# Kernel tuning notes

Hardware: AMD Instinct MI355X
Metric: run time of the kernel (lower is better)

The kernel has to match this reference:

```python
import jax, jax.numpy as jnp
import numpy as np

EPS = 1e-5
GRID = 128          # coarse grid extent -> fine grid is 256^3
N1 = 15000          # coarse voxels
CHILD = 4           # children kept per coarse voxel
N2 = N1 * CHILD     # fine voxels
CIN = 128
COUT = 64


def _build_geometry():
    rng = np.random.RandomState(0)
    flat = rng.choice(GRID ** 3, N1, replace=False)
    cc = np.stack(np.unravel_index(flat, (GRID, GRID, GRID)), axis=1)  # [N1,3]
    offs8 = np.array([[i, j, k] for i in (0, 1) for j in (0, 1) for k in (0, 1)], dtype=np.int64)
    kidx = np.argsort(rng.rand(N1, 8), axis=1)[:, :CHILD]              # [N1,4] distinct child taps
    fine = (cc[:, None, :] * 2 + offs8[kidx]).reshape(-1, 3)           # [N2,3] unique fine coords
    up_src = np.repeat(np.arange(N1), CHILD).astype(np.int32)
    up_kidx = kidx.reshape(-1).astype(np.int32)
    # 27-offset neighbor maps via hashed coordinate lookup
    key = (fine[:, 0] * 256 + fine[:, 1]) * 256 + fine[:, 2]
    order = np.argsort(key)
    skey = key[order]
    offs27 = np.array([[i, j, k] for i in (-1, 0, 1) for j in (-1, 0, 1) for k in (-1, 0, 1)], dtype=np.int64)
    nbr_src = np.full((27, N2), N2, dtype=np.int32)
    nbr_dst = np.full((27, N2), N2, dtype=np.int32)
    for t in range(27):
        q = fine + offs27[t]
        inb = np.all((q >= 0) & (q < 256), axis=1)
        qk = (q[:, 0] * 256 + q[:, 1]) * 256 + q[:, 2]
        pos = np.searchsorted(skey, qk)
        pos = np.clip(pos, 0, N2 - 1)
        hit = inb & (skey[pos] == qk)
        nbr_src[t, hit] = order[pos[hit]]
        nbr_dst[t, hit] = np.arange(N2, dtype=np.int32)[hit]
    return up_src, up_kidx, nbr_src, nbr_dst


def setup_inputs() -> dict:
    key = jax.random.key(0)
    ks = jax.random.split(key, 8)
    up_src, up_kidx, nbr_src, nbr_dst = _build_geometry()
    s_up = 1.0 / np.sqrt(CIN * 8)
    s1 = 1.0 / np.sqrt(CIN * 27)
    s2 = 1.0 / np.sqrt(COUT * 27)
    return {
        "feats1": jax.random.normal(ks[0], (N1, CIN), jnp.float32),
        "feats2": jax.random.normal(ks[1], (N2, CIN // 2), jnp.float32),
        "w_up": jax.random.normal(ks[2], (8, CIN, CIN // 2), jnp.float32) * s_up,
        "gamma_up": jnp.ones((CIN // 2,), jnp.float32),
        "beta_up": jnp.zeros((CIN // 2,), jnp.float32),
        "w1": jax.random.normal(ks[3], (27, CIN, COUT), jnp.float32) * s1,
        "gamma1": jnp.ones((COUT,), jnp.float32),
        "beta1": jnp.zeros((COUT,), jnp.float32),
        "w2": jax.random.normal(ks[4], (27, COUT, COUT), jnp.float32) * s2,
        "gamma2": jnp.ones((COUT,), jnp.float32),
        "beta2": jnp.zeros((COUT,), jnp.float32),
        "up_src": jnp.asarray(up_src),
        "up_kidx": jnp.asarray(up_kidx),
        "nbr_src": jnp.asarray(nbr_src),
        "nbr_dst": jnp.asarray(nbr_dst),
    }


def _bn_relu(x, gamma, beta):
    # training-mode BatchNorm over the point dimension (biased variance), then ReLU
    m = jnp.mean(x, axis=0)
    v = jnp.var(x, axis=0)
    return jax.nn.relu((x - m) * jax.lax.rsqrt(v + EPS) * gamma + beta)


def _sparse_conv(x, w, nbr_src, nbr_dst):
    # x: [N,Ci]; w: [27,Ci,Co]; transform-then-gather-scatter (hash-map sparse conv)
    n = x.shape[0]
    co = w.shape[-1]
    y = jnp.einsum("nc,kco->kno", x, w)                       # [27,N,Co]
    y = jnp.concatenate([y, jnp.zeros((27, 1, co), y.dtype)], axis=1)  # sentinel row
    msg = jnp.take_along_axis(y, nbr_src[:, :, None], axis=1)  # [27,N,Co]
    out = jnp.zeros((n + 1, co), y.dtype).at[nbr_dst.reshape(-1)].add(msg.reshape(-1, co))
    return out[:-1]


def reference(feats1, feats2, w_up, gamma_up, beta_up, w1, gamma1, beta1, w2,
              gamma2, beta2, up_src, up_kidx, nbr_src, nbr_dst):
    # transposed conv k=2 s=2, generative=False: each fine voxel pulls from its unique coarse parent
    y = jnp.einsum("mc,kco->kmo", feats1, w_up)               # [8,N1,Cin/2]
    x1 = y[up_kidx, up_src]                                   # [N2,Cin/2]
    x1 = _bn_relu(x1, gamma_up, beta_up)
    x = jnp.concatenate([x1, feats2], axis=-1)                # [N2,Cin]
    h = _bn_relu(_sparse_conv(x, w1, nbr_src, nbr_dst), gamma1, beta1)
    return _bn_relu(_sparse_conv(h, w2, nbr_src, nbr_dst), gamma2, beta2)
```

## Files before the change

kernel.cpp:

```cpp
#include <hip/hip_runtime.h>


typedef short bf16x4 __attribute__((ext_vector_type(4)));
typedef short bf16x8 __attribute__((ext_vector_type(8)));
typedef float f32x16 __attribute__((ext_vector_type(16)));

#define ROWM 0xFFFFF
#define RFLAG (1 << 30)

__device__ __forceinline__ short f2bf(float f) {
    unsigned u = __float_as_uint(f);
    u += 0x7fffu + ((u >> 16) & 1u);
    return (short)(u >> 16);
}
__device__ __forceinline__ float bf2f(short s) {
    return __uint_as_float(((unsigned)(unsigned short)s) << 16);
}

__global__ __launch_bounds__(256) void k_setup(
    const float* __restrict__ w_up, const float* __restrict__ f1,
    const int* __restrict__ up_kidx,
    short* __restrict__ wupp, short* __restrict__ f1bf,
    int* __restrict__ pmask, int* __restrict__ perm_rows,
    int* __restrict__ rank, int* __restrict__ cnt,
    int n1, int nbGeom)
{
    int tid = threadIdx.x;
    int bid = blockIdx.x;
    if (bid < nbGeom) {
        int p = bid * 256 + tid;
        if (p >= n1) return;
        int4 kd = *(const int4*)(up_kidx + 4 * p);
        int a = kd.x * 4 + 0, b = kd.y * 4 + 1, c = kd.z * 4 + 2, d = kd.w * 4 + 3;
        int t;
        if (a > b) { t = a; a = b; b = t; }
        if (c > d) { t = c; c = d; d = t; }
        if (a > c) { t = a; a = c; c = t; }
        if (b > d) { t = b; b = d; d = t; }
        if (b > c) { t = b; b = c; c = t; }
        perm_rows[4 * p + 0] = 4 * p + (a & 3);
        perm_rows[4 * p + 1] = 4 * p + (b & 3);
        perm_rows[4 * p + 2] = 4 * p + (c & 3);
        perm_rows[4 * p + 3] = 4 * p + (d & 3);
        int mask = (1 << (a >> 2)) | (1 << (b >> 2)) | (1 << (c >> 2)) | (1 << (d >> 2));
        pmask[p] = mask;
        rank[p] = atomicAdd(&cnt[mask], 1);
    } else {
        const int nup8 = 8192;
        int tot = nup8 + n1 * 16;
        int gs = (gridDim.x - nbGeom) * 256;
        for (int e8 = (bid - nbGeom) * 256 + tid; e8 < tot; e8 += gs) {
            if (e8 < nup8) {
                int l = e8 & 63, nt = (e8 >> 6) & 15, ks = e8 >> 10;
                int kb = ks * 16 + (l >> 5) * 8;
                int col = nt * 32 + (l & 31);
                const float* src = w_up + (size_t)(col >> 6) * 8192 + (size_t)kb * 64 + (col & 63);
                bf16x8 o;
                #pragma unroll
                for (int j = 0; j < 8; ++j) o[j] = f2bf(src[(size_t)j * 64]);
                *(bf16x8*)(wupp + (size_t)e8 * 8) = o;
            } else {
                int g = e8 - nup8;
                const float* src = f1 + (size_t)g * 8;
                float4 a = *(const float4*)src;
                float4 b = *(const float4*)(src + 4);
                bf16x8 o;
                o[0] = f2bf(a.x); o[1] = f2bf(a.y); o[2] = f2bf(a.z); o[3] = f2bf(a.w);
                o[4] = f2bf(b.x); o[5] = f2bf(b.y); o[6] = f2bf(b.z); o[7] = f2bf(b.w);
                *(bf16x8*)(f1bf + (size_t)g * 8) = o;
            }
        }
    }
}

__global__ __launch_bounds__(256) void k_up(
    const short* __restrict__ f1bf, const short* __restrict__ wupp,
    const int* __restrict__ pmask, const int* __restrict__ cnt,
    const int* __restrict__ rank, int* __restrict__ perm_par,
    int4* __restrict__ tiles, int* __restrict__ ntl,
    short* __restrict__ yup8, float* __restrict__ stats,
    const float* __restrict__ w1, const float* __restrict__ w2,
    short* __restrict__ w1p, short* __restrict__ w2p,
    const int* __restrict__ nbr, int2* __restrict__ ext,
    int* __restrict__ extc, unsigned* __restrict__ flagbits,
    float* __restrict__ y1, float* __restrict__ y2,
    int n1, int n2, int nt, int nbExt)
{
    int gemmEnd = 1 + 2 * nt;
    if (blockIdx.x == 0) {
        __shared__ int sA[256], sB[256], bb[256];
        int t = threadIdx.x;
        int c = cnt[t], tc = (c + 31) >> 5;
        sA[t] = c; sB[t] = tc;
        __syncthreads();
        for (int off = 1; off < 256; off <<= 1) {
            int a = (t >= off) ? sA[t - off] : 0;
            int b = (t >= off) ? sB[t - off] : 0;
            __syncthreads();
            sA[t] += a; sB[t] += b;
            __syncthreads();
        }
        int base = sA[t] - c, toff = sB[t] - tc;
        bb[t] = base;
        for (int j = 0; j < tc; ++j) tiles[toff + j] = make_int4(t, base, j * 32, c);
        if (t == 255) ntl[0] = sB[255];
        __syncthreads();
        for (int p = t; p < n1; p += 256)
            perm_par[bb[pmask[p]] + rank[p]] = p;
        return;
    }
    if (blockIdx.x >= gemmEnd) {
        int ab = blockIdx.x - gemmEnd;
        int tid = threadIdx.x;
        if (ab < 256) {
            long long tot = (long long)n2 * 16;
            float4 z = make_float4(0.f, 0.f, 0.f, 0.f);
            for (long long e = (long long)ab * 256 + tid; e < tot; e += 256LL * 256) {
                ((float4*)y1)[e] = z;
                ((float4*)y2)[e] = z;
            }
        } else if (ab < 320) {
            const int nw18 = 27648, tot = 27648 + 13824;
            for (int e8 = (ab - 256) * 256 + tid; e8 < tot; e8 += 64 * 256) {
                if (e8 < nw18) {
                    int l = e8 & 63, ch = (e8 >> 6) & 1, ks = (e8 >> 7) & 7, t = e8 >> 10;
                    int kb = ks * 16 + (l >> 5) * 8;
                    int col = ch * 32 + (l & 31);
                    const float* src = w1 + (size_t)t * 8192 + (size_t)kb * 64 + col;
                    bf16x8 o;
                    #pragma unroll
                    for (int j = 0; j < 8; ++j) o[j] = f2bf(src[(size_t)j * 64]);
                    *(bf16x8*)(w1p + (size_t)e8 * 8) = o;
                } else {
                    int g = e8 - nw18;
                    int l = g & 63, ch = (g >> 6) & 1, ks = (g >> 7) & 3, t = g >> 9;
                    int kb = ks * 16 + (l >> 5) * 8;
                    int col = ch * 32 + (l & 31);
                    const float* src = w2 + (size_t)t * 4096 + (size_t)kb * 64 + col;
                    bf16x8 o;
                    #pragma unroll
                    for (int j = 0; j < 8; ++j) o[j] = f2bf(src[(size_t)j * 64]);
                    *(bf16x8*)(w2p + (size_t)g * 8) = o;
                }
            }
        } else {
            int i = (ab - 320) * 256 + tid;
            unsigned hm = 0;
            if (i < n2) {
                #pragma unroll
                for (int t = 0; t < 27; ++t) {
                    int s = nbr[(size_t)t * n2 + i];
                    if (s < n2 && (s >> 2) != (i >> 2)) hm |= 1u << t;
                }
            }
            if (hm) atomicOr(&flagbits[i >> 5], 1u << (i & 31));
            __shared__ int lcnt, lbase;
            if (tid == 0) lcnt = 0;
            __syncthreads();
            int nh = __popc(hm);
            int myofs = 0;
            if (nh) myofs = atomicAdd(&lcnt, nh);
            __syncthreads();
            if (tid == 0 && lcnt) lbase = atomicAdd(extc, lcnt);
            __syncthreads();
            if (nh) {
                int pos = lbase + myofs;
                unsigned m = hm;
                while (m) {
                    int t = __ffs(m) - 1;
                    m &= m - 1;
                    int s = nbr[(size_t)t * n2 + i];
                    ext[pos++] = make_int2(i, s | (t << 16));
                }
            }
        }
        return;
    }
    __shared__ short lds[32 * 136];
    __shared__ float bs[64], bq[64];
    int bid = blockIdx.x - 1;
    int tile = bid >> 1;
    int w = threadIdx.x >> 6, lane = threadIdx.x & 63;
    int na = (bid & 1) * 8 + w, nb = na + 4;
    if (threadIdx.x < 64) { bs[threadIdx.x] = 0.f; bq[threadIdx.x] = 0.f; }
    #pragma unroll
    for (int it = 0; it < 2; ++it) {
        int c = it * 256 + threadIdx.x;
        int row = c >> 4, col8 = c & 15;
        int gr = tile * 32 + row; if (gr >= n1) gr = n1 - 1;
        int4 g = *(const int4*)(f1bf + (size_t)gr * 128 + col8 * 8);
        short* d = &lds[row * 136 + col8 * 8];
        *(int2*)d = make_int2(g.x, g.y);
        *(int2*)(d + 4) = make_int2(g.z, g.w);
    }
    int m = lane & 31, half = lane >> 5;
    int pm_l = (tile * 32 + m < n1) ? pmask[tile * 32 + m] : 0;
    __syncthreads();
    f32x16 a0, a1;
    #pragma unroll
    for (int i = 0; i < 16; ++i) { a0[i] = 0.f; a1[i] = 0.f; }
    const bf16x8* bp = (const bf16x8*)wupp;
    #pragma unroll
    for (int ks = 0; ks < 8; ++ks) {
        const short* ap = &lds[m * 136 + ks * 16 + half * 8];
        bf16x4 lo = *(const bf16x4*)ap, hi = *(const bf16x4*)(ap + 4);
        bf16x8 a = __builtin_shufflevector(lo, hi, 0, 1, 2, 3, 4, 5, 6, 7);
        bf16x8 b0 = bp[(size_t)(ks * 16 + na) * 64 + lane];
        bf16x8 b1 = bp[(size_t)(ks * 16 + nb) * 64 + lane];
        a0 = __builtin_amdgcn_mfma_f32_32x32x16_bf16(a, b0, a0, 0, 0, 0);
        a1 = __builtin_amdgcn_mfma_f32_32x32x16_bf16(a, b1, a1, 0, 0, 0);
    }
    int col = lane & 31;
    #pragma unroll
    for (int pass = 0; pass < 2; ++pass) {
        const f32x16& acc = pass ? a1 : a0;
        int n = pass ? nb : na;
        int slot = n >> 1, c = (n & 1) * 32 + col;
        float s0 = 0.f, q0 = 0.f;
        #pragma unroll
        for (int reg = 0; reg < 16; ++reg) {
            int r = (reg & 3) + 8 * (reg >> 2) + 4 * half;
            int p = tile * 32 + r;
            float v = acc[reg];
            int mk = __shfl(pm_l, r);
            if (p < n1) {
                yup8[(size_t)p * 512 + n * 32 + col] = f2bf(v);
                if ((mk >> slot) & 1) { s0 += v; q0 += v * v; }
            }
        }
        s0 += __shfl_xor(s0, 32);
        q0 += __shfl_xor(q0, 32);
        if (lane < 32) { atomicAdd(&bs[c], s0); atomicAdd(&bq[c], q0); }
    }
    __syncthreads();
    if (threadIdx.x < 64) {
        atomicAdd(&stats[threadIdx.x], bs[threadIdx.x]);
        atomicAdd(&stats[64 + threadIdx.x], bq[threadIdx.x]);
    }
}

__device__ __forceinline__ void pair_epi2(const f32x16& a0v, const f32x16& a1v,
                                          int outrow0, int outrow1, int lane,
                                          int ch, float* __restrict__ y,
                                          float* __restrict__ bs,
                                          float* __restrict__ bq)
{
    int col = lane & 31;
    int c = ch * 32 + col;
    float s0 = 0.f, q0 = 0.f;
    #pragma unroll
    for (int reg = 0; reg < 16; ++reg) {
        int r = (reg & 3) + 8 * (reg >> 2) + 4 * (lane >> 5);
        int r0 = __shfl(outrow0, r);
        int r1 = __shfl(outrow1, r);
        if (r0 >= 0) {
            float v = a0v[reg];
            size_t ad = (size_t)(r0 & ROWM) * 64 + c;
            if (r0 & RFLAG) {
                float old = atomicAdd(&y[ad], v);
                s0 += v; q0 += v * (v + 2.f * old);
            } else {
                y[ad] = v; s0 += v; q0 += v * v;
            }
        }
        if (r1 >= 0) {
            float v = a1v[reg];
            size_t ad = (size_t)(r1 & ROWM) * 64 + c;
            if (r1 & RFLAG) {
                float old = atomicAdd(&y[ad], v);
                s0 += v; q0 += v * (v + 2.f * old);
            } else {
                y[ad] = v; s0 += v; q0 += v * v;
            }
        }
    }
    s0 += __shfl_xor(s0, 32);
    q0 += __shfl_xor(q0, 32);
    if (lane < 32) { atomicAdd(&bs[c], s0); atomicAdd(&bq[c], q0); }
}

__device__ __forceinline__ int tap27(int pa, int pb) {
    int di = ((pb >> 2) & 1) - ((pa >> 2) & 1);
    int dj = ((pb >> 1) & 1) - ((pa >> 1) & 1);
    int dk = (pb & 1) - (pa & 1);
    return (di + 1) * 9 + (dj + 1) * 3 + (dk + 1);
}

__global__ __launch_bounds__(256) void k_pairA(
    const short* __restrict__ yup8, const float* __restrict__ f2,
    const int* __restrict__ up_kidx, const short* __restrict__ wp,
    const float* __restrict__ gamma, const float* __restrict__ beta,
    const float* __restrict__ stats, const int* __restrict__ perm_par,
    const int* __restrict__ perm_rows, const int4* __restrict__ tiles,
    const int* __restrict__ n_tiles, const int2* __restrict__ ext,
    const int* __restrict__ extc, const unsigned* __restrict__ flagbits,
    float* __restrict__ y, float* __restrict__ ostats, int n2, int nExtB)
{
    constexpr int LP = 520;
    __shared__ short lds[32 * LP];
    __shared__ int srows[128], soff[128];
    __shared__ float scs[64], shs[64], bs[64], bq[64];
    int tid = threadIdx.x;
    if (blockIdx.x < nExtB) {
        if (tid < 64) {
            float inv = 1.0f / (float)n2;
            float mean = stats[tid] * inv;
            float var = stats[64 + tid] * inv - mean * mean;
            float s = gamma[tid] * rsqrtf(var + 1e-5f);
            scs[tid] = s; shs[tid] = beta[tid] - mean * s;
            bs[tid] = 0.f; bq[tid] = 0.f;
        }
        __syncthreads();
        int gw = (blockIdx.x * 256 + tid) >> 6;
        int nw = nExtB * 4;
        int c = tid & 63;
        int ch = c >> 5, lcol = c & 31;
        int ec = extc[0];
        const bf16x8* wb = (const bf16x8*)wp;
        for (int e = gw; e < ec; e += nw) {
            int2 en = ext[e];
            int i = en.x, s = en.y & 0xFFFF, t = en.y >> 16;
            const short* xr = yup8 + (size_t)(s >> 2) * 512 + up_kidx[s] * 64;
            const float* fr = f2 + (size_t)s * 64;
            float acc = 0.f;
            #pragma unroll
            for (int ks = 0; ks < 8; ++ks) {
                #pragma unroll
                for (int hf = 0; hf < 2; ++hf) {
                    int kb = ks * 16 + hf * 8;
                    float xv[8];
                    if (kb < 64) {
                        bf16x8 g = *(const bf16x8*)(xr + kb);
                        #pragma unroll
                        for (int j = 0; j < 8; ++j)
                            xv[j] = fmaxf(bf2f(g[j]) * scs[kb + j] + shs[kb + j], 0.f);
                    } else {
                        float4 g0 = *(const float4*)(fr + kb - 64);
                        float4 g1 = *(const float4*)(fr + kb - 60);
                        xv[0] = g0.x; xv[1] = g0.y; xv[2] = g0.z; xv[3] = g0.w;
                        xv[4] = g1.x; xv[5] = g1.y; xv[6] = g1.z; xv[7] = g1.w;
                    }
                    bf16x8 wv = wb[((size_t)(t * 8 + ks) * 2 + ch) * 64 + hf * 32 + lcol];
                    #pragma unroll
                    for (int j = 0; j < 8; ++j)
                        acc += xv[j] * bf2f(wv[j]);
                }
            }
            float old = atomicAdd(&y[(size_t)i * 64 + c], acc);
            atomicAdd(&bs[c], acc);
            atomicAdd(&bq[c], acc * (acc + 2.f * old));
        }
        __syncthreads();
        if (tid < 64) {
            atomicAdd(&ostats[tid], bs[tid]);
            atomicAdd(&ostats[64 + tid], bq[tid]);
        }
        return;
    }
    int bt = blockIdx.x - nExtB;
    if (bt >= n_tiles[0]) return;
    int4 td = tiles[bt];
    int mask = td.x, p_start = td.y, lt = td.z, cntb = td.w;
    if (tid < 128) {
        int li = lt + (tid >> 2);
        int pid = perm_par[p_start + ((li < cntb) ? li : 0)];
        int i = perm_rows[pid * 4 + (tid & 3)];
        unsigned fb = (flagbits[i >> 5] >> (i & 31)) & 1u;
        srows[tid] = i | (int)(fb << 30);
        soff[tid] = (i >> 2) * 512 + up_kidx[i] * 64;
    } else if (tid < 192) {
        int cc = tid - 128;
        float inv = 1.0f / (float)n2;
        float mean = stats[cc] * inv;
        float var = stats[64 + cc] * inv - mean * mean;
        float s = gamma[cc] * rsqrtf(var + 1e-5f);
        scs[cc] = s; shs[cc] = beta[cc] - mean * s;
    } else {
        int cc = tid - 192;
        bs[cc] = 0.f; bq[cc] = 0.f;
    }
    __syncthreads();
    #pragma unroll
    for (int it = 0; it < 8; ++it) {
        int c0 = it * 256 + tid;
        int pl = c0 >> 6, w8 = c0 & 63;
        int j = w8 >> 4, col8 = w8 & 15;
        short* d = &lds[pl * LP + j * 128 + col8 * 8];
        if (col8 < 8) {
            bf16x8 g = *(const bf16x8*)(yup8 + (size_t)soff[pl * 4 + j] + col8 * 8);
            short o[8];
            #pragma unroll
            for (int u = 0; u < 8; ++u) {
                int cc = col8 * 8 + u;
                o[u] = f2bf(fmaxf(bf2f(g[u]) * scs[cc] + shs[cc], 0.f));
            }
            *(int2*)d = make_int2(((int)(unsigned short)o[0]) | ((int)o[1] << 16),
                                  ((int)(unsigned short)o[2]) | ((int)o[3] << 16));
            *(int2*)(d + 4) = make_int2(((int)(unsigned short)o[4]) | ((int)o[5] << 16),
                                        ((int)(unsigned short)o[6]) | ((int)o[7] << 16));
        } else {
            const float* fr = f2 + (size_t)(srows[pl * 4 + j] & ROWM) * 64 + (col8 - 8) * 8;
            float4 f0 = *(const float4*)fr;
            float4 f1v = *(const float4*)(fr + 4);
            short o[8] = {f2bf(f0.x), f2bf(f0.y), f2bf(f0.z), f2bf(f0.w),
                          f2bf(f1v.x), f2bf(f1v.y), f2bf(f1v.z), f2bf(f1v.w)};
            *(int2*)d = make_int2(((int)(unsigned short)o[0]) | ((int)o[1] << 16),
                                  ((int)(unsigned short)o[2]) | ((int)o[3] << 16));
            *(int2*)(d + 4) = make_int2(((int)(unsigned short)o[4]) | ((int)o[5] << 16),
                                        ((int)(unsigned short)o[6]) | ((int)o[7] << 16));
        }
    }
    int p0 = -1, p1 = -1, p2 = -1, p3 = -1;
    #pragma unroll
    for (int b = 7; b >= 0; --b)
        if ((mask >> b) & 1) { p3 = p2; p2 = p1; p1 = p0; p0 = b; }
    int w = tid >> 6, lane = tid & 63;
    int a0 = w >> 1, a1 = a0 + 2, ch = w & 1;
    int pa0 = (a0 == 0) ? p0 : p1;
    int pa1 = (a1 == 2) ? p2 : p3;
    int t00 = tap27(pa0, p0), t01 = tap27(pa0, p1), t02 = tap27(pa0, p2), t03 = tap27(pa0, p3);
    int t10 = tap27(pa1, p0), t11 = tap27(pa1, p1), t12 = tap27(pa1, p2), t13 = tap27(pa1, p3);
    int m = lane & 31, half = lane >> 5;
    int li = lt + m;
    bool vp = li < cntb;
    int outrow0 = vp ? srows[m * 4 + a0] : -1;
    int outrow1 = vp ? srows[m * 4 + a1] : -1;
    __syncthreads();
    f32x16 acc0, acc1;
    #pragma unroll
    for (int i = 0; i < 16; ++i) { acc0[i] = 0.f; acc1[i] = 0.f; }
    const bf16x8* bp = (const bf16x8*)wp;
    #pragma unroll
    for (int b = 0; b < 4; ++b) {
        int tb0 = (b == 0) ? t00 : (b == 1) ? t01 : (b == 2) ? t02 : t03;
        int tb1 = (b == 0) ? t10 : (b == 1) ? t11 : (b == 2) ? t12 : t13;
        #pragma unroll
        for (int kk = 0; kk < 8; ++kk) {
            int ks = b * 8 + kk;
            const short* ap = &lds[m * LP + ks * 16 + half * 8];
            bf16x4 lo = *(const bf16x4*)ap, hi = *(const bf16x4*)(ap + 4);
            bf16x8 a = __builtin_shufflevector(lo, hi, 0, 1, 2, 3, 4, 5, 6, 7);
            bf16x8 b0 = bp[((size_t)(tb0 * 8 + kk) * 2 + ch) * 64 + lane];
            bf16x8 b1 = bp[((size_t)(tb1 * 8 + kk) * 2 + ch) * 64 + lane];
            acc0 = __builtin_amdgcn_mfma_f32_32x32x16_bf16(a, b0, acc0, 0, 0, 0);
            acc1 = __builtin_amdgcn_mfma_f32_32x32x16_bf16(a, b1, acc1, 0, 0, 0);
        }
    }
    pair_epi2(acc0, acc1, outrow0, outrow1, lane, ch, y, bs, bq);
    __syncthreads();
    if (tid < 64) {
        atomicAdd(&ostats[tid], bs[tid]);
        atomicAdd(&ostats[64 + tid], bq[tid]);
    }
}

__global__ __launch_bounds__(256) void k_pairB(
    const float* __restrict__ y1, const short* __restrict__ wp,
    const float* __restrict__ gamma, const float* __restrict__ beta,
    const float* __restrict__ stats, const int* __restrict__ perm_par,
    const int* __restrict__ perm_rows, const int4* __restrict__ tiles,
    const int* __restrict__ n_tiles, const int2* __restrict__ ext,
    const int* __restrict__ extc, const unsigned* __restrict__ flagbits,
    float* __restrict__ y, float* __restrict__ ostats, int n2, int nExtB)
{
    constexpr int LP = 264;
    __shared__ short lds[32 * LP];
    __shared__ int srows[128];
    __shared__ float scs[64], shs[64], bs[64], bq[64];
    int tid = threadIdx.x;
    if (blockIdx.x < nExtB) {
        if (tid < 64) {
            float inv = 1.0f / (float)n2;
            float mean = stats[tid] * inv;
            float var = stats[64 + tid] * inv - mean * mean;
            float s = gamma[tid] * rsqrtf(var + 1e-5f);
            scs[tid] = s; shs[tid] = beta[tid] - mean * s;
            bs[tid] = 0.f; bq[tid] = 0.f;
        }
        __syncthreads();
        int gw = (blockIdx.x * 256 + tid) >> 6;
        int nw = nExtB * 4;
        int c = tid & 63;
        int ch = c >> 5, lcol = c & 31;
        int ec = extc[0];
        const bf16x8* wb = (const bf16x8*)wp;
        for (int e = gw; e < ec; e += nw) {
            int2 en = ext[e];
            int i = en.x, s = en.y & 0xFFFF, t = en.y >> 16;
            const float* hr = y1 + (size_t)s * 64;
            float acc = 0.f;
            #pragma unroll
            for (int ks = 0; ks < 4; ++ks) {
                #pragma unroll
                for (int hf = 0; hf < 2; ++hf) {
                    int kb = ks * 16 + hf * 8;
                    float4 g0 = *(const float4*)(hr + kb);
                    float4 g1 = *(const float4*)(hr + kb + 4);
                    float xv[8];
                    xv[0] = g0.x; xv[1] = g0.y; xv[2] = g0.z; xv[3] = g0.w;
                    xv[4] = g1.x; xv[5] = g1.y; xv[6] = g1.z; xv[7] = g1.w;
                    #pragma unroll
                    for (int j = 0; j < 8; ++j)
                        xv[j] = fmaxf(xv[j] * scs[kb + j] + shs[kb + j], 0.f);
                    bf16x8 wv = wb[((size_t)(t * 4 + ks) * 2 + ch) * 64 + hf * 32 + lcol];
                    #pragma unroll
                    for (int j = 0; j < 8; ++j)
                        acc += xv[j] * bf2f(wv[j]);
                }
            }
            float old = atomicAdd(&y[(size_t)i * 64 + c], acc);
            atomicAdd(&bs[c], acc);
            atomicAdd(&bq[c], acc * (acc + 2.f * old));
        }
        __syncthreads();
        if (tid < 64) {
            atomicAdd(&ostats[tid], bs[tid]);
            atomicAdd(&ostats[64 + tid], bq[tid]);
        }
        return;
    }
    int bt = blockIdx.x - nExtB;
    if (bt >= n_tiles[0]) return;
    int4 td = tiles[bt];
    int mask = td.x, p_start = td.y, lt = td.z, cntb = td.w;
    if (tid < 128) {
        int li = lt + (tid >> 2);
        int pid = perm_par[p_start + ((li < cntb) ? li : 0)];
        int i = perm_rows[pid * 4 + (tid & 3)];
        unsigned fb = (flagbits[i >> 5] >> (i & 31)) & 1u;
        srows[tid] = i | (int)(fb << 30);
    } else if (tid < 192) {
        int cc = tid - 128;
        float inv = 1.0f / (float)n2;
        float mean = stats[cc] * inv;
        float var = stats[64 + cc] * inv - mean * mean;
        float s = gamma[cc] * rsqrtf(var + 1e-5f);
        scs[cc] = s; shs[cc] = beta[cc] - mean * s;
    } else {
        int cc = tid - 192;
        bs[cc] = 0.f; bq[cc] = 0.f;
    }
    __syncthreads();
    #pragma unroll
    for (int it = 0; it < 4; ++it) {
        int c0 = it * 256 + tid;
        int pl = c0 >> 5, w8 = c0 & 31;
        int j = w8 >> 3, col8 = w8 & 7;
        const float* fr = y1 + (size_t)(srows[pl * 4 + j] & ROWM) * 64 + col8 * 8;
        float4 f0 = *(const float4*)fr;
        float4 f1v = *(const float4*)(fr + 4);
        short o[8];
        #pragma unroll
        for (int u = 0; u < 4; ++u) {
            int cc = col8 * 8 + u;
            float v = (u == 0) ? f0.x : (u == 1) ? f0.y : (u == 2) ? f0.z : f0.w;
            o[u] = f2bf(fmaxf(v * scs[cc] + shs[cc], 0.f));
        }
        #pragma unroll
        for (int u = 0; u < 4; ++u) {
            int cc = col8 * 8 + 4 + u;
            float v = (u == 0) ? f1v.x : (u == 1) ? f1v.y : (u == 2) ? f1v.z : f1v.w;
            o[4 + u] = f2bf(fmaxf(v * scs[cc] + shs[cc], 0.f));
        }
        short* d = &lds[pl * LP + j * 64 + col8 * 8];
        *(int2*)d = make_int2(((int)(unsigned short)o[0]) | ((int)o[1] << 16),
                              ((int)(unsigned short)o[2]) | ((int)o[3] << 16));
        *(int2*)(d + 4) = make_int2(((int)(unsigned short)o[4]) | ((int)o[5] << 16),
                                    ((int)(unsigned short)o[6]) | ((int)o[7] << 16));
    }
    int p0 = -1, p1 = -1, p2 = -1, p3 = -1;
    #pragma unroll
    for (int b = 7; b >= 0; --b)
        if ((mask >> b) & 1) { p3 = p2; p2 = p1; p1 = p0; p0 = b; }
    int w = tid >> 6, lane = tid & 63;
    int a0 = w >> 1, a1 = a0 + 2, ch = w & 1;
    int pa0 = (a0 == 0) ? p0 : p1;
    int pa1 = (a1 == 2) ? p2 : p3;
    int t00 = tap27(pa0, p0), t01 = tap27(pa0, p1), t02 = tap27(pa0, p2), t03 = tap27(pa0, p3);
    int t10 = tap27(pa1, p0), t11 = tap27(pa1, p1), t12 = tap27(pa1, p2), t13 = tap27(pa1, p3);
    int m = lane & 31, half = lane >> 5;
    int li = lt + m;
    bool vp = li < cntb;
    int outrow0 = vp ? srows[m * 4 + a0] : -1;
    int outrow1 = vp ? srows[m * 4 + a1] : -1;
    __syncthreads();
    f32x16 acc0, acc1;
    #pragma unroll
    for (int i = 0; i < 16; ++i) { acc0[i] = 0.f; acc1[i] = 0.f; }
    const bf16x8* bp = (const bf16x8*)wp;
    #pragma unroll
    for (int b = 0; b < 4; ++b) {
        int tb0 = (b == 0) ? t00 : (b == 1) ? t01 : (b == 2) ? t02 : t03;
        int tb1 = (b == 0) ? t10 : (b == 1) ? t11 : (b == 2) ? t12 : t13;
        #pragma unroll
        for (int kk = 0; kk < 4; ++kk) {
            int ks = b * 4 + kk;
            const short* ap = &lds[m * LP + ks * 16 + half * 8];
            bf16x4 lo = *(const bf16x4*)ap, hi = *(const bf16x4*)(ap + 4);
            bf16x8 a = __builtin_shufflevector(lo, hi, 0, 1, 2, 3, 4, 5, 6, 7);
            bf16x8 b0 = bp[((size_t)(tb0 * 4 + kk) * 2 + ch) * 64 + lane];
            bf16x8 b1 = bp[((size_t)(tb1 * 4 + kk) * 2 + ch) * 64 + lane];
            acc0 = __builtin_amdgcn_mfma_f32_32x32x16_bf16(a, b0, acc0, 0, 0, 0);
            acc1 = __builtin_amdgcn_mfma_f32_32x32x16_bf16(a, b1, acc1, 0, 0, 0);
        }
    }
    pair_epi2(acc0, acc1, outrow0, outrow1, lane, ch, y, bs, bq);
    __syncthreads();
    if (tid < 64) {
        atomicAdd(&ostats[tid], bs[tid]);
        atomicAdd(&ostats[64 + tid], bq[tid]);
    }
}

__global__ __launch_bounds__(256) void k_final(
    const float* __restrict__ y, const float* __restrict__ gamma,
    const float* __restrict__ beta, const float* __restrict__ stats,
    float* __restrict__ out, int n2)
{
    __shared__ float sc[64], sh[64];
    int tid = threadIdx.x;
    if (tid < 64) {
        float inv = 1.0f / (float)n2;
        float mean = stats[tid] * inv;
        float var = stats[64 + tid] * inv - mean * mean;
        float s = gamma[tid] * rsqrtf(var + 1e-5f);
        sc[tid] = s;
        sh[tid] = beta[tid] - mean * s;
    }
    __syncthreads();
    long long total = (long long)n2 * 16;
    long long stride = (long long)gridDim.x * blockDim.x;
    for (long long idx = (long long)blockIdx.x * blockDim.x + tid; idx < total; idx += stride) {
        int i = (int)(idx >> 4);
        int c4 = ((int)idx & 15) * 4;
        const float* src = y + (size_t)i * 64 + c4;
        float4 o;
        o.x = fmaxf(src[0] * sc[c4 + 0] + sh[c4 + 0], 0.f);
        o.y = fmaxf(src[1] * sc[c4 + 1] + sh[c4 + 1], 0.f);
        o.z = fmaxf(src[2] * sc[c4 + 2] + sh[c4 + 2], 0.f);
        o.w = fmaxf(src[3] * sc[c4 + 3] + sh[c4 + 3], 0.f);
        *(float4*)(out + (size_t)i * 64 + c4) = o;
    }
}

extern "C" void kernel_launch(void* const* d_in, const int* in_sizes, int n_in,
                              void* d_out, int out_size, void* d_ws, size_t ws_size,
                              hipStream_t stream)
{
    const float* feats1   = (const float*)d_in[0];
    const float* feats2   = (const float*)d_in[1];
    const float* w_up     = (const float*)d_in[2];
    const float* gamma_up = (const float*)d_in[3];
    const float* beta_up  = (const float*)d_in[4];
    const float* w1       = (const float*)d_in[5];
    const float* gamma1   = (const float*)d_in[6];
    const float* beta1    = (const float*)d_in[7];
    const float* w2       = (const float*)d_in[8];
    const float* gamma2   = (const float*)d_in[9];
    const float* beta2    = (const float*)d_in[10];
    const int* up_src     = (const int*)d_in[11];  (void)up_src;
    const int* up_kidx    = (const int*)d_in[12];
    const int* nbr_src    = (const int*)d_in[13];

    int n1 = in_sizes[0] / 128;
    int n2 = in_sizes[1] / 64;

    char* p = (char*)d_ws;
    auto alloc = [&](size_t bytes) {
        char* r = p;
        p += (bytes + 255) & ~(size_t)255;
        return r;
    };
    float* stats    = (float*)alloc(384 * 4);
    int*   cnt      = (int*)alloc(256 * 4);
    int*   extc     = (int*)alloc(16);
    int*   ntl      = (int*)alloc(16);
    unsigned* flagbits = (unsigned*)alloc(((size_t)(n2 + 31) / 32) * 4);
    size_t headBytes = (size_t)(p - (char*)d_ws);
    int maxTiles    = (n1 + 31) / 32 + 80;
    int4*  tiles    = (int4*)alloc((size_t)maxTiles * 16);
    short* wupp     = (short*)alloc((size_t)65536 * 2);
    short* w1p      = (short*)alloc((size_t)221184 * 2);
    short* w2p      = (short*)alloc((size_t)110592 * 2);
    short* f1bf     = (short*)alloc((size_t)n1 * 128 * 2);
    int*   pmask    = (int*)alloc((size_t)n1 * 4);
    int*   rank     = (int*)alloc((size_t)n1 * 4);
    int*   perm_par = (int*)alloc((size_t)n1 * 4);
    int*   perm_rows= (int*)alloc((size_t)4 * n1 * 4);
    int2*  ext      = (int2*)alloc((size_t)27 * n2 * 8);
    short* yup8     = (short*)alloc((size_t)n1 * 512 * 2);
    float* y1       = (float*)alloc((size_t)n2 * 64 * 4);
    float* y2       = (float*)alloc((size_t)n2 * 64 * 4);

    int nbExt  = (n2 + 255) / 256;
    int nbGeom = (n1 + 255) / 256;
    int nbPack = 128;
    int nbSetup = nbGeom + nbPack;
    int nt = (n1 + 31) / 32;
    int upBlocks = 1 + 2 * nt + 256 + 64 + nbExt;
    int ewBlocks16 = (int)(((long long)n2 * 16 + 255) / 256);
    const int EXTB = 256;

    hipMemsetAsync(d_ws, 0, headBytes, stream);
    k_setup<<<nbSetup, 256, 0, stream>>>(w_up, feats1, up_kidx, wupp, f1bf,
                                         pmask, perm_rows, rank, cnt,
                                         n1, nbGeom);
    k_up<<<upBlocks, 256, 0, stream>>>(f1bf, wupp, pmask, cnt, rank, perm_par,
                                       tiles, ntl, yup8, stats,
                                       w1, w2, w1p, w2p, nbr_src, ext, extc,
                                       flagbits, y1, y2, n1, n2, nt, nbExt);
    k_pairA<<<EXTB + maxTiles, 256, 0, stream>>>(yup8, feats2, up_kidx, w1p,
                                                 gamma_up, beta_up, stats,
                                                 perm_par, perm_rows, tiles, ntl,
                                                 ext, extc, flagbits,
                                                 y1, stats + 128, n2, EXTB);
    k_pairB<<<EXTB + maxTiles, 256, 0, stream>>>(y1, w2p, gamma1, beta1,
                                                 stats + 128, perm_par,
                                                 perm_rows, tiles, ntl,
                                                 ext, extc, flagbits,
                                                 y2, stats + 256, n2, EXTB);
    k_final<<<ewBlocks16, 256, 0, stream>>>(y2, gamma2, beta2, stats + 256,
                                            (float*)d_out, n2);
}
```

Baseline: 232.7 us.

## Use 512-thread blocks with one output row-slot per wave in pair kernels

The pair convolution kernels move from 256 to 512 threads, so each of the 8 waves computes a single output sub-position (one accumulator) instead of two per wave. Extra-edge blocks are halved so the total number of gather waves stays the same. This shortens each wave's serial MFMA chain and the atomic epilogue, and it doubles the waves sharing each LDS tile. In exchange, every wave reloads the A tile from LDS, and larger blocks with the same LDS footprint may change occupancy.

```diff
diff --git a/kernel.cpp b/kernel.cpp
--- a/kernel.cpp
+++ b/kernel.cpp
@@ -239,9 +239,9 @@
     }
 }
 
-__device__ __forceinline__ void pair_epi2(const f32x16& a0v, const f32x16& a1v,
-                                          int outrow0, int outrow1, int lane,
-                                          int ch, float* __restrict__ y,
+__device__ __forceinline__ void pair_epi1(const f32x16& av, int outrow,
+                                          int lane, int ch,
+                                          float* __restrict__ y,
                                           float* __restrict__ bs,
                                           float* __restrict__ bq)
 {
@@ -251,10 +251,9 @@
     #pragma unroll
     for (int reg = 0; reg < 16; ++reg) {
         int r = (reg & 3) + 8 * (reg >> 2) + 4 * (lane >> 5);
-        int r0 = __shfl(outrow0, r);
-        int r1 = __shfl(outrow1, r);
+        int r0 = __shfl(outrow, r);
         if (r0 >= 0) {
-            float v = a0v[reg];
+            float v = av[reg];
             size_t ad = (size_t)(r0 & ROWM) * 64 + c;
             if (r0 & RFLAG) {
                 float old = atomicAdd(&y[ad], v);
@@ -263,16 +262,6 @@
                 y[ad] = v; s0 += v; q0 += v * v;
             }
         }
-        if (r1 >= 0) {
-            float v = a1v[reg];
-            size_t ad = (size_t)(r1 & ROWM) * 64 + c;
-            if (r1 & RFLAG) {
-                float old = atomicAdd(&y[ad], v);
-                s0 += v; q0 += v * (v + 2.f * old);
-            } else {
-                y[ad] = v; s0 += v; q0 += v * v;
-            }
-        }
     }
     s0 += __shfl_xor(s0, 32);
     q0 += __shfl_xor(q0, 32);
@@ -286,7 +275,7 @@
     return (di + 1) * 9 + (dj + 1) * 3 + (dk + 1);
 }
 
-__global__ __launch_bounds__(256) void k_pairA(
+__global__ __launch_bounds__(512) void k_pairA(
     const short* __restrict__ yup8, const float* __restrict__ f2,
     const int* __restrict__ up_kidx, const short* __restrict__ wp,
     const float* __restrict__ gamma, const float* __restrict__ beta,
@@ -311,8 +300,8 @@
             bs[tid] = 0.f; bq[tid] = 0.f;
         }
         __syncthreads();
-        int gw = (blockIdx.x * 256 + tid) >> 6;
-        int nw = nExtB * 4;
+        int gw = (blockIdx.x * 512 + tid) >> 6;
+        int nw = nExtB * 8;
         int c = tid & 63;
         int ch = c >> 5, lcol = c & 31;
         int ec = extc[0];
@@ -375,14 +364,14 @@
         float var = stats[64 + cc] * inv - mean * mean;
         float s = gamma[cc] * rsqrtf(var + 1e-5f);
         scs[cc] = s; shs[cc] = beta[cc] - mean * s;
-    } else {
+    } else if (tid < 256) {
         int cc = tid - 192;
         bs[cc] = 0.f; bq[cc] = 0.f;
     }
     __syncthreads();
     #pragma unroll
-    for (int it = 0; it < 8; ++it) {
-        int c0 = it * 256 + tid;
+    for (int it = 0; it < 4; ++it) {
+        int c0 = it * 512 + tid;
         int pl = c0 >> 6, w8 = c0 & 63;
         int j = w8 >> 4, col8 = w8 & 15;
         short* d = &lds[pl * LP + j * 128 + col8 * 8];
@@ -415,38 +404,32 @@
     for (int b = 7; b >= 0; --b)
         if ((mask >> b) & 1) { p3 = p2; p2 = p1; p1 = p0; p0 = b; }
     int w = tid >> 6, lane = tid & 63;
-    int a0 = w >> 1, a1 = a0 + 2, ch = w & 1;
-    int pa0 = (a0 == 0) ? p0 : p1;
-    int pa1 = (a1 == 2) ? p2 : p3;
-    int t00 = tap27(pa0, p0), t01 = tap27(pa0, p1), t02 = tap27(pa0, p2), t03 = tap27(pa0, p3);
-    int t10 = tap27(pa1, p0), t11 = tap27(pa1, p1), t12 = tap27(pa1, p2), t13 = tap27(pa1, p3);
+    int asub = w >> 1, ch = w & 1;
+    int pa = (asub == 0) ? p0 : (asub == 1) ? p1 : (asub == 2) ? p2 : p3;
+    int t0 = tap27(pa, p0), t1 = tap27(pa, p1), t2 = tap27(pa, p2), t3 = tap27(pa, p3);
     int m = lane & 31, half = lane >> 5;
     int li = lt + m;
     bool vp = li < cntb;
-    int outrow0 = vp ? srows[m * 4 + a0] : -1;
-    int outrow1 = vp ? srows[m * 4 + a1] : -1;
-    __syncthreads();
-    f32x16 acc0, acc1;
-    #pragma unroll
-    for (int i = 0; i < 16; ++i) { acc0[i] = 0.f; acc1[i] = 0.f; }
+    int outrow = vp ? srows[m * 4 + asub] : -1;
+    __syncthreads();
+    f32x16 acc;
+    #pragma unroll
+    for (int i = 0; i < 16; ++i) acc[i] = 0.f;
     const bf16x8* bp = (const bf16x8*)wp;
     #pragma unroll
     for (int b = 0; b < 4; ++b) {
-        int tb0 = (b == 0) ? t00 : (b == 1) ? t01 : (b == 2) ? t02 : t03;
-        int tb1 = (b == 0) ? t10 : (b == 1) ? t11 : (b == 2) ? t12 : t13;
+        int tb = (b == 0) ? t0 : (b == 1) ? t1 : (b == 2) ? t2 : t3;
         #pragma unroll
         for (int kk = 0; kk < 8; ++kk) {
             int ks = b * 8 + kk;
             const short* ap = &lds[m * LP + ks * 16 + half * 8];
             bf16x4 lo = *(const bf16x4*)ap, hi = *(const bf16x4*)(ap + 4);
             bf16x8 a = __builtin_shufflevector(lo, hi, 0, 1, 2, 3, 4, 5, 6, 7);
-            bf16x8 b0 = bp[((size_t)(tb0 * 8 + kk) * 2 + ch) * 64 + lane];
-            bf16x8 b1 = bp[((size_t)(tb1 * 8 + kk) * 2 + ch) * 64 + lane];
-            acc0 = __builtin_amdgcn_mfma_f32_32x32x16_bf16(a, b0, acc0, 0, 0, 0);
-            acc1 = __builtin_amdgcn_mfma_f32_32x32x16_bf16(a, b1, acc1, 0, 0, 0);
-        }
-    }
-    pair_epi2(acc0, acc1, outrow0, outrow1, lane, ch, y, bs, bq);
+            bf16x8 b0 = bp[((size_t)(tb * 8 + kk) * 2 + ch) * 64 + lane];
+            acc = __builtin_amdgcn_mfma_f32_32x32x16_bf16(a, b0, acc, 0, 0, 0);
+        }
+    }
+    pair_epi1(acc, outrow, lane, ch, y, bs, bq);
     __syncthreads();
     if (tid < 64) {
         atomicAdd(&ostats[tid], bs[tid]);
@@ -454,7 +437,7 @@
     }
 }
 
-__global__ __launch_bounds__(256) void k_pairB(
+__global__ __launch_bounds__(512) void k_pairB(
     const float* __restrict__ y1, const short* __restrict__ wp,
     const float* __restrict__ gamma, const float* __restrict__ beta,
     const float* __restrict__ stats, const int* __restrict__ perm_par,
@@ -478,8 +461,8 @@
             bs[tid] = 0.f; bq[tid] = 0.f;
         }
         __syncthreads();
-        int gw = (blockIdx.x * 256 + tid) >> 6;
-        int nw = nExtB * 4;
+        int gw = (blockIdx.x * 512 + tid) >> 6;
+        int nw = nExtB * 8;
         int c = tid & 63;
         int ch = c >> 5, lcol = c & 31;
         int ec = extc[0];
@@ -536,14 +519,14 @@
         float var = stats[64 + cc] * inv - mean * mean;
         float s = gamma[cc] * rsqrtf(var + 1e-5f);
         scs[cc] = s; shs[cc] = beta[cc] - mean * s;
-    } else {
+    } else if (tid < 256) {
         int cc = tid - 192;
         bs[cc] = 0.f; bq[cc] = 0.f;
     }
     __syncthreads();
     #pragma unroll
-    for (int it = 0; it < 4; ++it) {
-        int c0 = it * 256 + tid;
+    for (int it = 0; it < 2; ++it) {
+        int c0 = it * 512 + tid;
         int pl = c0 >> 5, w8 = c0 & 31;
         int j = w8 >> 3, col8 = w8 & 7;
         const float* fr = y1 + (size_t)(srows[pl * 4 + j] & ROWM) * 64 + col8 * 8;
@@ -573,38 +556,32 @@
     for (int b = 7; b >= 0; --b)
         if ((mask >> b) & 1) { p3 = p2; p2 = p1; p1 = p0; p0 = b; }
     int w = tid >> 6, lane = tid & 63;
-    int a0 = w >> 1, a1 = a0 + 2, ch = w & 1;
-    int pa0 = (a0 == 0) ? p0 : p1;
-    int pa1 = (a1 == 2) ? p2 : p3;
-    int t00 = tap27(pa0, p0), t01 = tap27(pa0, p1), t02 = tap27(pa0, p2), t03 = tap27(pa0, p3);
-    int t10 = tap27(pa1, p0), t11 = tap27(pa1, p1), t12 = tap27(pa1, p2), t13 = tap27(pa1, p3);
+    int asub = w >> 1, ch = w & 1;
+    int pa = (asub == 0) ? p0 : (asub == 1) ? p1 : (asub == 2) ? p2 : p3;
+    int t0 = tap27(pa, p0), t1 = tap27(pa, p1), t2 = tap27(pa, p2), t3 = tap27(pa, p3);
     int m = lane & 31, half = lane >> 5;
     int li = lt + m;
     bool vp = li < cntb;
-    int outrow0 = vp ? srows[m * 4 + a0] : -1;
-    int outrow1 = vp ? srows[m * 4 + a1] : -1;
-    __syncthreads();
-    f32x16 acc0, acc1;
-    #pragma unroll
-    for (int i = 0; i < 16; ++i) { acc0[i] = 0.f; acc1[i] = 0.f; }
+    int outrow = vp ? srows[m * 4 + asub] : -1;
+    __syncthreads();
+    f32x16 acc;
+    #pragma unroll
+    for (int i = 0; i < 16; ++i) acc[i] = 0.f;
     const bf16x8* bp = (const bf16x8*)wp;
     #pragma unroll
     for (int b = 0; b < 4; ++b) {
-        int tb0 = (b == 0) ? t00 : (b == 1) ? t01 : (b == 2) ? t02 : t03;
-        int tb1 = (b == 0) ? t10 : (b == 1) ? t11 : (b == 2) ? t12 : t13;
+        int tb = (b == 0) ? t0 : (b == 1) ? t1 : (b == 2) ? t2 : t3;
         #pragma unroll
         for (int kk = 0; kk < 4; ++kk) {
             int ks = b * 4 + kk;
             const short* ap = &lds[m * LP + ks * 16 + half * 8];
             bf16x4 lo = *(const bf16x4*)ap, hi = *(const bf16x4*)(ap + 4);
             bf16x8 a = __builtin_shufflevector(lo, hi, 0, 1, 2, 3, 4, 5, 6, 7);
-            bf16x8 b0 = bp[((size_t)(tb0 * 4 + kk) * 2 + ch) * 64 + lane];
-            bf16x8 b1 = bp[((size_t)(tb1 * 4 + kk) * 2 + ch) * 64 + lane];
-            acc0 = __builtin_amdgcn_mfma_f32_32x32x16_bf16(a, b0, acc0, 0, 0, 0);
-            acc1 = __builtin_amdgcn_mfma_f32_32x32x16_bf16(a, b1, acc1, 0, 0, 0);
-        }
-    }
-    pair_epi2(acc0, acc1, outrow0, outrow1, lane, ch, y, bs, bq);
+            bf16x8 b0 = bp[((size_t)(tb * 4 + kk) * 2 + ch) * 64 + lane];
+            acc = __builtin_amdgcn_mfma_f32_32x32x16_bf16(a, b0, acc, 0, 0, 0);
+        }
+    }
+    pair_epi1(acc, outrow, lane, ch, y, bs, bq);
     __syncthreads();
     if (tid < 64) {
         atomicAdd(&ostats[tid], bs[tid]);
@@ -699,7 +676,7 @@
     int nt = (n1 + 31) / 32;
     int upBlocks = 1 + 2 * nt + 256 + 64 + nbExt;
     int ewBlocks16 = (int)(((long long)n2 * 16 + 255) / 256);
-    const int EXTB = 256;
+    const int EXTB = 128;
 
     hipMemsetAsync(d_ws, 0, headBytes, stream);
     k_setup<<<nbSetup, 256, 0, stream>>>(w_up, feats1, up_kidx, wupp, f1bf,
@@ -709,12 +686,12 @@
                                        tiles, ntl, yup8, stats,
                                        w1, w2, w1p, w2p, nbr_src, ext, extc,
                                        flagbits, y1, y2, n1, n2, nt, nbExt);
-    k_pairA<<<EXTB + maxTiles, 256, 0, stream>>>(yup8, feats2, up_kidx, w1p,
+    k_pairA<<<EXTB + maxTiles, 512, 0, stream>>>(yup8, feats2, up_kidx, w1p,
                                                  gamma_up, beta_up, stats,
                                                  perm_par, perm_rows, tiles, ntl,
                                                  ext, extc, flagbits,
                                                  y1, stats + 128, n2, EXTB);
-    k_pairB<<<EXTB + maxTiles, 256, 0, stream>>>(y1, w2p, gamma1, beta1,
+    k_pairB<<<EXTB + maxTiles, 512, 0, stream>>>(y1, w2p, gamma1, beta1,
                                                  stats + 128, perm_par,
                                                  perm_rows, tiles, ntl,
                                                  ext, extc, flagbits,
```

Result: faster. 226.4 us (median of 2 runs) (-2.7%).
